# Kernel optimization log

Hardware: AMD Instinct MI355X
Metric: run time of the kernel (lower is better)

## Reference

```python
import jax, jax.numpy as jnp
import numpy as np
from jax import lax

PADDING_L = 30  # causal: kernel_size - 1


def setup_inputs() -> dict:
    key = jax.random.key(0)
    k1, k2 = jax.random.split(key)
    T, B, C = 4096, 8, 1024
    H, K = 16, 31
    x = jax.random.normal(k1, (T, B, C), dtype=jnp.float32)
    weight = jax.random.normal(k2, (H, K), dtype=jnp.float32)
    return {"x": x, "weight": weight}


def reference(x, weight):
    # x: [T, B, C]; weight: [H, K]
    T, B, C = x.shape
    H, K = weight.shape
    R = C // H  # channels per head share the same kernel
    # weight_softmax=True: normalize kernel taps per head
    w = jax.nn.softmax(weight, axis=-1)            # [H, K]
    wc = jnp.repeat(w, R, axis=0)[:, None, :]      # [C, 1, K] depthwise kernel
    xb = jnp.transpose(x, (1, 2, 0))               # [B, C, T]
    # lightconv_cuda: out[b,c,t] = sum_k w[h(c),k] * x_pad[b,c,t+k],
    # left pad = padding_l, right pad = K-1-padding_l (cross-correlation)
    out = lax.conv_general_dilated(
        xb, wc,
        window_strides=(1,),
        padding=[(PADDING_L, K - 1 - PADDING_L)],
        feature_group_count=C,
        dimension_numbers=("NCH", "OIH", "NCH"),
    )                                              # [B, C, T]
    return jnp.transpose(out, (2, 0, 1))           # [T, B, C]
```

## Files before the change

### kernel.cpp

```cpp
#include <hip/hip_runtime.h>
#include <math.h>

#define T_DIM 4096
#define B_DIM 8
#define C_DIM 1024
#define H_DIM 16
#define K_DIM 31
#define PAD_L 30
#define TILE_T 32
#define WIN (TILE_T + PAD_L)
#define BLOCK 256

__global__ __launch_bounds__(BLOCK, 2) void lightconv_kernel(
    const float* __restrict__ x,
    const float* __restrict__ w,
    float* __restrict__ out)
{
    __shared__ float s_taps[4][K_DIM];

    const int tid    = threadIdx.x;
    const int colBlk = blockIdx.x;
    const int tBlk   = blockIdx.y;
    const int cc     = colBlk * BLOCK + tid;
    const int t0     = tBlk * TILE_T;

    if (tid < 4) {
        const int c0 = (colBlk * BLOCK) % C_DIM;
        const int h  = (c0 >> 6) + tid;
        const float* wr = w + h * K_DIM;
        float m = -1e30f;
        #pragma unroll
        for (int k = 0; k < K_DIM; ++k) m = fmaxf(m, wr[k]);
        float s = 0.0f;
        #pragma unroll
        for (int k = 0; k < K_DIM; ++k) {
            float e = __expf(wr[k] - m);
            s_taps[tid][k] = e;
            s += e;
        }
        const float inv = 1.0f / s;
        #pragma unroll
        for (int k = 0; k < K_DIM; ++k) s_taps[tid][k] *= inv;
    }
    __syncthreads();

    const int hl = tid >> 6;
    float taps[K_DIM];
    #pragma unroll
    for (int k = 0; k < K_DIM; ++k) {
        taps[k] = __int_as_float(
            __builtin_amdgcn_readfirstlane(__float_as_int(s_taps[hl][k])));
    }

    const long stride = (long)B_DIM * C_DIM;

    float xv[WIN];
    const float* px = x + (long)(t0 - PAD_L) * stride + cc;
    if (t0 >= PAD_L) {
        #pragma unroll
        for (int j = 0; j < WIN; ++j) xv[j] = px[(long)j * stride];
    } else {
        #pragma unroll
        for (int j = 0; j < WIN; ++j)
            xv[j] = (j >= PAD_L) ? px[(long)j * stride] : 0.0f;
    }

    __builtin_amdgcn_sched_barrier(0);

    float* po = out + (long)t0 * stride + cc;
    #pragma unroll
    for (int i = 0; i < TILE_T; ++i) {
        float a0 = 0.0f, a1 = 0.0f, a2 = 0.0f, a3 = 0.0f;
        #pragma unroll
        for (int k = 0; k < 8; ++k)  a0 = fmaf(taps[k],      xv[i + k],      a0);
        #pragma unroll
        for (int k = 0; k < 8; ++k)  a1 = fmaf(taps[8 + k],  xv[i + 8 + k],  a1);
        #pragma unroll
        for (int k = 0; k < 8; ++k)  a2 = fmaf(taps[16 + k], xv[i + 16 + k], a2);
        #pragma unroll
        for (int k = 0; k < 7; ++k)  a3 = fmaf(taps[24 + k], xv[i + 24 + k], a3);
        __builtin_nontemporal_store((a0 + a1) + (a2 + a3), po + (long)i * stride);
    }
}

extern "C" void kernel_launch(void* const* d_in, const int* in_sizes, int n_in,
                              void* d_out, int out_size, void* d_ws, size_t ws_size,
                              hipStream_t stream) {
    const float* x = (const float*)d_in[0];
    const float* w = (const float*)d_in[1];
    float* out = (float*)d_out;

    dim3 grid((B_DIM * C_DIM) / BLOCK, T_DIM / TILE_T);
    lightconv_kernel<<<grid, BLOCK, 0, stream>>>(x, w, out);
}
```

Before: 234.6 us.

## Stage input window into LDS via global_load_lds and stream scatter-accumulate

Replaces per-thread strided global loads of the time window with 16-byte direct global-to-LDS transfers (global_load_lds) into a shared tile, with zero-fill for rows before the sequence start. The convolution becomes a scatter form: each input row is read once from LDS and FMA'd into up to 32 accumulators, which cuts the live input registers. This targets load latency and issue overhead and register pressure. The cost is a 62x256 float LDS tile per block, which can limit occupancy, plus the LDS read traffic.

```diff
diff --git a/kernel.cpp b/kernel.cpp
--- a/kernel.cpp
+++ b/kernel.cpp
@@ -8,21 +8,72 @@
 #define K_DIM 31
 #define PAD_L 30
 #define TILE_T 32
-#define WIN (TILE_T + PAD_L)
+#define WIN (TILE_T + K_DIM - 1)
 #define BLOCK 256
+
+typedef __attribute__((ext_vector_type(4))) float f32x4;
+
+__device__ __forceinline__ void stage16(const float* g, float* l) {
+    __builtin_amdgcn_global_load_lds(
+        (const __attribute__((address_space(1))) void*)g,
+        (__attribute__((address_space(3))) void*)l,
+        16, 0, 0);
+}
+
+template <int J>
+__device__ __forceinline__ void conv_step(const float* col,
+                                          const float (&taps)[K_DIM],
+                                          float (&acc)[TILE_T]) {
+    const float xj = col[J * BLOCK];
+    #pragma unroll
+    for (int i = 0; i < TILE_T; ++i) {
+        if (J - i >= 0 && J - i < K_DIM)
+            acc[i] = fmaf(taps[J - i], xj, acc[i]);
+    }
+}
+
+template <int J>
+__device__ __forceinline__ void conv_all(const float* col,
+                                         const float (&taps)[K_DIM],
+                                         float (&acc)[TILE_T]) {
+    if constexpr (J < WIN) {
+        conv_step<J>(col, taps, acc);
+        conv_all<J + 1>(col, taps, acc);
+    }
+}
 
 __global__ __launch_bounds__(BLOCK, 2) void lightconv_kernel(
     const float* __restrict__ x,
     const float* __restrict__ w,
     float* __restrict__ out)
 {
+    __shared__ float tile[WIN][BLOCK];
     __shared__ float s_taps[4][K_DIM];
 
     const int tid    = threadIdx.x;
+    const int lane   = tid & 63;
+    const int wv     = tid >> 6;
     const int colBlk = blockIdx.x;
     const int tBlk   = blockIdx.y;
-    const int cc     = colBlk * BLOCK + tid;
     const int t0     = tBlk * TILE_T;
+    const long stride = (long)B_DIM * C_DIM;
+
+    {
+        const float* gbase = x + (long)(t0 - PAD_L) * stride
+                               + colBlk * BLOCK + lane * 4;
+        #pragma unroll
+        for (int i = 0; i < 16; ++i) {
+            const int r = wv * 16 + i;
+            if (r < WIN) {
+                if (t0 - PAD_L + r >= 0) {
+                    stage16(gbase + (long)r * stride, &tile[r][0]);
+                } else {
+                    const f32x4 z = {0.0f, 0.0f, 0.0f, 0.0f};
+                    *(f32x4*)&tile[r][lane * 4] = z;
+                }
+            }
+        }
+    }
 
     if (tid < 4) {
         const int c0 = (colBlk * BLOCK) % C_DIM;
@@ -42,45 +93,26 @@
         #pragma unroll
         for (int k = 0; k < K_DIM; ++k) s_taps[tid][k] *= inv;
     }
+
     __syncthreads();
 
-    const int hl = tid >> 6;
     float taps[K_DIM];
     #pragma unroll
     for (int k = 0; k < K_DIM; ++k) {
         taps[k] = __int_as_float(
-            __builtin_amdgcn_readfirstlane(__float_as_int(s_taps[hl][k])));
+            __builtin_amdgcn_readfirstlane(__float_as_int(s_taps[wv][k])));
     }
 
-    const long stride = (long)B_DIM * C_DIM;
+    float acc[TILE_T];
+    #pragma unroll
+    for (int i = 0; i < TILE_T; ++i) acc[i] = 0.0f;
 
-    float xv[WIN];
-    const float* px = x + (long)(t0 - PAD_L) * stride + cc;
-    if (t0 >= PAD_L) {
-        #pragma unroll
-        for (int j = 0; j < WIN; ++j) xv[j] = px[(long)j * stride];
-    } else {
-        #pragma unroll
-        for (int j = 0; j < WIN; ++j)
-            xv[j] = (j >= PAD_L) ? px[(long)j * stride] : 0.0f;
-    }
+    conv_all<0>(&tile[0][0] + tid, taps, acc);
 
-    __builtin_amdgcn_sched_barrier(0);
-
-    float* po = out + (long)t0 * stride + cc;
+    float* po = out + (long)t0 * stride + (colBlk * BLOCK + tid);
     #pragma unroll
-    for (int i = 0; i < TILE_T; ++i) {
-        float a0 = 0.0f, a1 = 0.0f, a2 = 0.0f, a3 = 0.0f;
-        #pragma unroll
-        for (int k = 0; k < 8; ++k)  a0 = fmaf(taps[k],      xv[i + k],      a0);
-        #pragma unroll
-        for (int k = 0; k < 8; ++k)  a1 = fmaf(taps[8 + k],  xv[i + 8 + k],  a1);
-        #pragma unroll
-        for (int k = 0; k < 8; ++k)  a2 = fmaf(taps[16 + k], xv[i + 16 + k], a2);
-        #pragma unroll
-        for (int k = 0; k < 7; ++k)  a3 = fmaf(taps[24 + k], xv[i + 24 + k], a3);
-        __builtin_nontemporal_store((a0 + a1) + (a2 + a3), po + (long)i * stride);
-    }
+    for (int i = 0; i < TILE_T; ++i)
+        __builtin_nontemporal_store(acc[i], po + (long)i * stride);
 }
 
 extern "C" void kernel_launch(void* const* d_in, const int* in_sizes, int n_in,
```

Result: no change. 231.0 us (-1.5%).
